# Optimization experiments

Measured on AMD Instinct MI355X. Metric: run time of the kernel, lower is better.

## Reference

```python
import jax, jax.numpy as jnp
import numpy as np

T1 = 0.2
T2 = 1.2
LABEL_SMOOTHING = 0.05
NUM_ITERS = 20  # fixed-point iterations for lambda_t_a (t2 > 1 branch)


def log_t(x, t):
    # tempered log (t != 1)
    return (x ** (1.0 - t) - 1.0) / (1.0 - t)


def exp_t(x, t):
    # tempered exp (t != 1): relu((1-t)x + 1) ** (1/(1-t))
    return jnp.maximum((1.0 - t) * x + 1.0, 0.0) ** (1.0 / (1.0 - t))


def lambda_t_a(a, t):
    # t > 1 fixed-point branch of the original torch code, with a fixed
    # iteration count instead of a host-synced convergence check.
    mu = jnp.max(a, axis=-1, keepdims=True)            # [N, 1]
    norm_a_initial = a - mu                            # [N, C], <= 0

    def body(norm_a, _):
        z_a = jnp.sum(exp_t(norm_a, t), axis=-1, keepdims=True)  # [N, 1]
        return z_a ** (1.0 - t) * norm_a_initial, None

    norm_a, _ = jax.lax.scan(body, norm_a_initial, None, length=NUM_ITERS)
    z_a = jnp.sum(exp_t(norm_a, t), axis=-1, keepdims=True)
    return -log_t(1.0 / z_a, t) + mu                   # [N, 1]


def setup_inputs() -> dict:
    key = jax.random.key(0)
    k1, k2 = jax.random.split(key)
    N, C = 16384, 1000
    inputs = jax.random.normal(k1, (N, C), dtype=jnp.float32)
    labels = jax.random.randint(k2, (N,), 0, C)
    targets = jax.nn.one_hot(labels, C, dtype=jnp.float32)
    return {"inputs": inputs, "targets": targets}


def reference(inputs, targets):
    num_classes = targets.shape[-1]
    # label smoothing (label_smoothing > 0 branch)
    targets = (1.0 - num_classes / (num_classes - 1) * LABEL_SMOOTHING) * targets \
              + LABEL_SMOOTHING / (num_classes - 1)
    norm_constants = lambda_t_a(inputs, T2)                      # [N, 1]
    probabilities = exp_t(inputs - norm_constants, T2)           # [N, C]
    loss1 = targets * (log_t(targets + 1e-8, T1) - log_t(probabilities, T1))
    loss2 = (targets ** (2.0 - T1) - probabilities ** (2.0 - T1)) / (2.0 - T1)
    out = jnp.sum(loss1 - loss2, axis=-1)                        # [N]
    return jnp.mean(out)
```

## Files before the change

### kernel.cpp

```cpp
#include <hip/hip_runtime.h>
#include <math.h>

#define C_DIM 1000
#define BIG   1.0e30f

__device__ __forceinline__ float fexp2(float x) { return __builtin_amdgcn_exp2f(x); }
__device__ __forceinline__ float flog2(float x) { return __builtin_amdgcn_logf(x); }
__device__ __forceinline__ float frcp(float x)  { return __builtin_amdgcn_rcpf(x); }

template <int CTRL, int RM>
__device__ __forceinline__ float dpp_add_term(float x) {
    int y = __builtin_amdgcn_update_dpp(0, __float_as_int(x), CTRL, RM, 0xf, true);
    return __int_as_float(y);
}
template <int CTRL, int RM>
__device__ __forceinline__ float dpp_max_term(float x) {
    int y = __builtin_amdgcn_update_dpp(__float_as_int(x), __float_as_int(x), CTRL, RM, 0xf, false);
    return __int_as_float(y);
}

#define DPP_SUM_CHAIN(x)                      \
    x += dpp_add_term<0x111, 0xf>(x);         \
    x += dpp_add_term<0x112, 0xf>(x);         \
    x += dpp_add_term<0x114, 0xf>(x);         \
    x += dpp_add_term<0x118, 0xf>(x);         \
    x += dpp_add_term<0x142, 0xa>(x);         \
    x += dpp_add_term<0x143, 0xc>(x);

__device__ __forceinline__ float bcast63(float x) {
    return __int_as_float(__builtin_amdgcn_readlane(__float_as_int(x), 63));
}

__device__ __forceinline__ float wave_sum(float x) {
    DPP_SUM_CHAIN(x)
    return bcast63(x);
}

__device__ __forceinline__ float wave_max(float x) {
    x = fmaxf(x, dpp_max_term<0x111, 0xf>(x));
    x = fmaxf(x, dpp_max_term<0x112, 0xf>(x));
    x = fmaxf(x, dpp_max_term<0x114, 0xf>(x));
    x = fmaxf(x, dpp_max_term<0x118, 0xf>(x));
    x = fmaxf(x, dpp_max_term<0x142, 0xa>(x));
    x = fmaxf(x, dpp_max_term<0x143, 0xc>(x));
    return bcast63(x);
}

__device__ __forceinline__ float tr16(const float4 x0, const float4 x1,
                                      const float4 x2, const float4 x3,
                                      float bb[16])
{
    bb[0]=-0.2f*x0.x;  bb[1]=-0.2f*x0.y;  bb[2]=-0.2f*x0.z;  bb[3]=-0.2f*x0.w;
    bb[4]=-0.2f*x1.x;  bb[5]=-0.2f*x1.y;  bb[6]=-0.2f*x1.z;  bb[7]=-0.2f*x1.w;
    bb[8]=-0.2f*x2.x;  bb[9]=-0.2f*x2.y;  bb[10]=-0.2f*x2.z; bb[11]=-0.2f*x2.w;
    bb[12]=-0.2f*x3.x; bb[13]=-0.2f*x3.y; bb[14]=-0.2f*x3.z; bb[15]=-0.2f*x3.w;
    float m0 = fmaxf(fmaxf(x0.x, x0.y), fmaxf(x0.z, x0.w));
    float m1 = fmaxf(fmaxf(x1.x, x1.y), fmaxf(x1.z, x1.w));
    float m2 = fmaxf(fmaxf(x2.x, x2.y), fmaxf(x2.z, x2.w));
    float m3 = fmaxf(fmaxf(x3.x, x3.y), fmaxf(x3.z, x3.w));
    return fmaxf(fmaxf(m0, m1), fmaxf(m2, m3));
}

__device__ __forceinline__ float dot16(const float4 t0, const float4 t1,
                                       const float4 t2, const float4 t3,
                                       const float bb[16])
{
    float s = 0.0f;
    s = fmaf(t0.x, bb[0],  s); s = fmaf(t0.y, bb[1],  s);
    s = fmaf(t0.z, bb[2],  s); s = fmaf(t0.w, bb[3],  s);
    s = fmaf(t1.x, bb[4],  s); s = fmaf(t1.y, bb[5],  s);
    s = fmaf(t1.z, bb[6],  s); s = fmaf(t1.w, bb[7],  s);
    s = fmaf(t2.x, bb[8],  s); s = fmaf(t2.y, bb[9],  s);
    s = fmaf(t2.z, bb[10], s); s = fmaf(t2.w, bb[11], s);
    s = fmaf(t3.x, bb[12], s); s = fmaf(t3.y, bb[13], s);
    s = fmaf(t3.z, bb[14], s); s = fmaf(t3.w, bb[15], s);
    return s;
}

__device__ __forceinline__ void row_core(const float bb[16], float mxl, float ahbl,
                                         float* __restrict__ row_out, int row, int lane,
                                         float C0, float E_off, float dE)
{
    const float mu  = wave_max(mxl);
    const float ahb = wave_sum(ahbl);
    const float g   = 0.2f * mu;
    const float hb  = ahb + g;

    const float c1 = 1.0f + g;
    float s = 0.0f;
    #pragma unroll
    for (int k = 0; k < 16; ++k) {
        float u = bb[k] + c1;
        float u2 = u * u;
        s += frcp(u2 * u2 * u);
    }
    s = wave_sum(s);
    const float lam = fexp2(-0.2f * flog2(s));

    const float c2 = fmaf(lam, g, 1.0f);
    s = 0.0f;
    #pragma unroll
    for (int k = 0; k < 16; ++k) {
        float u = fmaf(lam, bb[k], c2);
        float u2 = u * u;
        s += frcp(u2 * u2 * u);
    }
    s = wave_sum(s);
    const float w = fexp2(0.2f * flog2(s));

    const float c3 = w + g;
    float S4 = 0.0f, S5 = 0.0f, S6 = 0.0f, S9 = 0.0f, S10 = 0.0f, S11 = 0.0f;
    #pragma unroll
    for (int k = 0; k < 16; ++k) {
        float r  = frcp(bb[k] + c3);
        float r2 = r * r;
        float r4 = r2 * r2;
        float r5 = r4 * r;
        float r9 = r4 * r5;
        S4  += r4;
        S5  += r5;
        S6  += r5 * r;
        S9  += r9;
        S10 += r5 * r5;
        S11 += r9 * r2;
    }
    DPP_SUM_CHAIN(S4)
    DPP_SUM_CHAIN(S5)
    DPP_SUM_CHAIN(S6)
    DPP_SUM_CHAIN(S9)
    DPP_SUM_CHAIN(S10)
    DPP_SUM_CHAIN(S11)
    S4 = bcast63(S4);  S5 = bcast63(S5);  S6 = bcast63(S6);
    S9 = bcast63(S9);  S10 = bcast63(S10); S11 = bcast63(S11);

    const float d   = (S5 - 1.0f) * 0.2f * frcp(S6);
    const float w1  = w + d;
    const float d2  = d * d;
    const float S4c = S4 + fmaf(10.0f * d2, S6,  -4.0f * d * S5);
    const float S9c = S9 + fmaf(45.0f * d2, S11, -9.0f * d * S10);
    const float rh  = frcp(w1 + hb);
    const float rh2 = rh * rh;
    const float rh4 = rh2 * rh2;

    const float loss = fmaf(-E_off, S4c,
                       fmaf(-dE, rh4,
                       fmaf(1.0f / 1.8f, S9c, C0)));
    if (lane == 0) row_out[row] = loss;
}

__global__ __launch_bounds__(256, 8) void btll(
    const float* __restrict__ inputs, const float* __restrict__ targets,
    float* __restrict__ row_out, int n_rows,
    float C0, float E_off, float dE)
{
    const int lane = threadIdx.x & 63;
    const int wave = threadIdx.x >> 6;
    const int wid  = blockIdx.x * 4 + wave;
    int row0 = wid * 2;
    if (row0 >= n_rows) return;
    int row1 = row0 + 1;
    const bool has1 = row1 < n_rows;
    if (!has1) row1 = row0;

    const float4* in0 = (const float4*)(inputs  + (size_t)row0 * C_DIM);
    const float4* tg0 = (const float4*)(targets + (size_t)row0 * C_DIM);
    const float4* in1 = (const float4*)(inputs  + (size_t)row1 * C_DIM);
    const float4* tg1 = (const float4*)(targets + (size_t)row1 * C_DIM);
    const bool m3 = (lane + 192) < 250;
    const float4 xpad = make_float4(-BIG, -BIG, -BIG, -BIG);
    const float4 tpad = make_float4(0.f, 0.f, 0.f, 0.f);

    float4 a0 = in0[lane];
    float4 a1 = in0[lane + 64];
    float4 a2 = in0[lane + 128];
    float4 a3 = m3 ? in0[lane + 192] : xpad;
    float4 t0 = tg0[lane];
    float4 t1 = tg0[lane + 64];
    float4 t2 = tg0[lane + 128];
    float4 t3 = m3 ? tg0[lane + 192] : tpad;
    float4 p0 = in1[lane];
    float4 p1 = in1[lane + 64];
    float4 p2 = in1[lane + 128];
    float4 p3 = m3 ? in1[lane + 192] : xpad;

    float bbA[16];
    float mxA = tr16(a0, a1, a2, a3, bbA);
    float ahA = dot16(t0, t1, t2, t3, bbA);

    float4 q0 = tg1[lane];
    float4 q1 = tg1[lane + 64];
    float4 q2 = tg1[lane + 128];
    float4 q3 = m3 ? tg1[lane + 192] : tpad;

    float bbB[16];
    float mxB = tr16(p0, p1, p2, p3, bbB);
    float ahB = dot16(q0, q1, q2, q3, bbB);

    row_core(bbA, mxA, ahA, row_out, row0, lane, C0, E_off, dE);
    if (has1) row_core(bbB, mxB, ahB, row_out, row1, lane, C0, E_off, dE);
}

__global__ __launch_bounds__(1024) void reduce_mean(
    const float* __restrict__ row_out, float* __restrict__ out, int n)
{
    __shared__ double sm[16];
    const int lane = threadIdx.x & 63;
    const int wv   = threadIdx.x >> 6;
    const int n4   = n >> 2;
    const float4* r4 = (const float4*)row_out;
    double s = 0.0;
    for (int i = threadIdx.x; i < n4; i += 1024) {
        float4 v = r4[i];
        s += (double)v.x + (double)v.y + (double)v.z + (double)v.w;
    }
    if (threadIdx.x == 0)
        for (int i = n4 << 2; i < n; ++i) s += (double)row_out[i];
    #pragma unroll
    for (int off = 32; off > 0; off >>= 1) s += __shfl_xor(s, off, 64);
    if (lane == 0) sm[wv] = s;
    __syncthreads();
    if (wv == 0) {
        double t = (lane < 16) ? sm[lane] : 0.0;
        #pragma unroll
        for (int off = 32; off > 0; off >>= 1) t += __shfl_xor(t, off, 64);
        if (lane == 0) out[0] = (float)(t / (double)n);
    }
}

extern "C" void kernel_launch(void* const* d_in, const int* in_sizes, int n_in,
                              void* d_out, int out_size, void* d_ws, size_t ws_size,
                              hipStream_t stream) {
    const float* inputs  = (const float*)d_in[0];
    const float* targets = (const float*)d_in[1];
    float* out = (float*)d_out;

    const int N = in_sizes[0] / C_DIM;
    float* row_out = (float*)d_ws;

    const double ls    = 0.05;
    const double c1g_d = 1.0 - (1000.0 / 999.0) * ls;
    const double c2_d  = ls / 999.0;
    const float  tp_on_f  = (float)c1g_d + (float)c2_d;
    const float  tp_off_f = (float)c2_d;
    const double tp_on  = (double)tp_on_f;
    const double tp_off = (double)tp_off_f;
    const double A_on  = (pow(tp_on  + 1e-8, 0.8) - 1.0) / 0.8;
    const double A_off = (pow(tp_off + 1e-8, 0.8) - 1.0) / 0.8;
    const double B_on  = pow(tp_on,  1.8);
    const double B_off = pow(tp_off, 1.8);
    const double E_on_d  = 1.25 * tp_on;
    const double E_off_d = 1.25 * tp_off;
    const double F_on_d  = tp_on  * A_on  + E_on_d  - B_on  / 1.8;
    const double F_off_d = tp_off * A_off + E_off_d - B_off / 1.8;
    const double C0_d    = (C_DIM - 1) * F_off_d + F_on_d;
    const double dE_d    = E_on_d - E_off_d;

    dim3 grid((N + 7) / 8);
    btll<<<grid, 256, 0, stream>>>(inputs, targets, row_out, N,
                                   (float)C0_d, (float)E_off_d, (float)dE_d);
    reduce_mean<<<1, 1024, 0, stream>>>(row_out, out, N);
}
```

Measured before the change: 168.6 us.

## Process four rows per wave with software-pipelined prefetch of next row

```diff
diff --git a/kernel.cpp b/kernel.cpp
--- a/kernel.cpp
+++ b/kernel.cpp
@@ -79,7 +79,7 @@
 
 __device__ __forceinline__ void row_core(const float bb[16], float mxl, float ahbl,
                                          float* __restrict__ row_out, int row, int lane,
-                                         float C0, float E_off, float dE)
+                                         bool st, float C0, float E_off, float dE)
 {
     const float mu  = wave_max(mxl);
     const float ahb = wave_sum(ahbl);
@@ -145,10 +145,10 @@
     const float loss = fmaf(-E_off, S4c,
                        fmaf(-dE, rh4,
                        fmaf(1.0f / 1.8f, S9c, C0)));
-    if (lane == 0) row_out[row] = loss;
-}
-
-__global__ __launch_bounds__(256, 8) void btll(
+    if (st && lane == 0) row_out[row] = loss;
+}
+
+__global__ __launch_bounds__(256, 4) void btll(
     const float* __restrict__ inputs, const float* __restrict__ targets,
     float* __restrict__ row_out, int n_rows,
     float C0, float E_off, float dE)
@@ -156,16 +156,26 @@
     const int lane = threadIdx.x & 63;
     const int wave = threadIdx.x >> 6;
     const int wid  = blockIdx.x * 4 + wave;
-    int row0 = wid * 2;
-    if (row0 >= n_rows) return;
-    int row1 = row0 + 1;
-    const bool has1 = row1 < n_rows;
-    if (!has1) row1 = row0;
-
-    const float4* in0 = (const float4*)(inputs  + (size_t)row0 * C_DIM);
-    const float4* tg0 = (const float4*)(targets + (size_t)row0 * C_DIM);
-    const float4* in1 = (const float4*)(inputs  + (size_t)row1 * C_DIM);
-    const float4* tg1 = (const float4*)(targets + (size_t)row1 * C_DIM);
+    const int rbase = wid * 4;
+    if (rbase >= n_rows) return;
+
+    const int r0 = rbase;
+    const int r1 = min(rbase + 1, n_rows - 1);
+    const int r2 = min(rbase + 2, n_rows - 1);
+    const int r3 = min(rbase + 3, n_rows - 1);
+    const bool st1 = (rbase + 1) < n_rows;
+    const bool st2 = (rbase + 2) < n_rows;
+    const bool st3 = (rbase + 3) < n_rows;
+
+    const float4* in0 = (const float4*)(inputs  + (size_t)r0 * C_DIM);
+    const float4* tg0 = (const float4*)(targets + (size_t)r0 * C_DIM);
+    const float4* in1 = (const float4*)(inputs  + (size_t)r1 * C_DIM);
+    const float4* tg1 = (const float4*)(targets + (size_t)r1 * C_DIM);
+    const float4* in2 = (const float4*)(inputs  + (size_t)r2 * C_DIM);
+    const float4* tg2 = (const float4*)(targets + (size_t)r2 * C_DIM);
+    const float4* in3 = (const float4*)(inputs  + (size_t)r3 * C_DIM);
+    const float4* tg3 = (const float4*)(targets + (size_t)r3 * C_DIM);
+
     const bool m3 = (lane + 192) < 250;
     const float4 xpad = make_float4(-BIG, -BIG, -BIG, -BIG);
     const float4 tpad = make_float4(0.f, 0.f, 0.f, 0.f);
@@ -183,21 +193,47 @@
     float4 p2 = in1[lane + 128];
     float4 p3 = m3 ? in1[lane + 192] : xpad;
 
-    float bbA[16];
-    float mxA = tr16(a0, a1, a2, a3, bbA);
-    float ahA = dot16(t0, t1, t2, t3, bbA);
-
-    float4 q0 = tg1[lane];
-    float4 q1 = tg1[lane + 64];
-    float4 q2 = tg1[lane + 128];
-    float4 q3 = m3 ? tg1[lane + 192] : tpad;
-
-    float bbB[16];
-    float mxB = tr16(p0, p1, p2, p3, bbB);
-    float ahB = dot16(q0, q1, q2, q3, bbB);
-
-    row_core(bbA, mxA, ahA, row_out, row0, lane, C0, E_off, dE);
-    if (has1) row_core(bbB, mxB, ahB, row_out, row1, lane, C0, E_off, dE);
+    float bbA[16], bbB[16];
+    float mx, ah;
+
+    mx = tr16(a0, a1, a2, a3, bbA);
+    ah = dot16(t0, t1, t2, t3, bbA);
+    t0 = tg1[lane];
+    t1 = tg1[lane + 64];
+    t2 = tg1[lane + 128];
+    t3 = m3 ? tg1[lane + 192] : tpad;
+
+    row_core(bbA, mx, ah, row_out, r0, lane, true, C0, E_off, dE);
+
+    mx = tr16(p0, p1, p2, p3, bbB);
+    ah = dot16(t0, t1, t2, t3, bbB);
+    p0 = in2[lane];
+    p1 = in2[lane + 64];
+    p2 = in2[lane + 128];
+    p3 = m3 ? in2[lane + 192] : xpad;
+    t0 = tg2[lane];
+    t1 = tg2[lane + 64];
+    t2 = tg2[lane + 128];
+    t3 = m3 ? tg2[lane + 192] : tpad;
+
+    row_core(bbB, mx, ah, row_out, r1, lane, st1, C0, E_off, dE);
+
+    mx = tr16(p0, p1, p2, p3, bbA);
+    ah = dot16(t0, t1, t2, t3, bbA);
+    p0 = in3[lane];
+    p1 = in3[lane + 64];
+    p2 = in3[lane + 128];
+    p3 = m3 ? in3[lane + 192] : xpad;
+    t0 = tg3[lane];
+    t1 = tg3[lane + 64];
+    t2 = tg3[lane + 128];
+    t3 = m3 ? tg3[lane + 192] : tpad;
+
+    row_core(bbA, mx, ah, row_out, r2, lane, st2, C0, E_off, dE);
+
+    mx = tr16(p0, p1, p2, p3, bbB);
+    ah = dot16(t0, t1, t2, t3, bbB);
+    row_core(bbB, mx, ah, row_out, r3, lane, st3, C0, E_off, dE);
 }
 
 __global__ __launch_bounds__(1024) void reduce_mean(
@@ -255,7 +291,7 @@
     const double C0_d    = (C_DIM - 1) * F_off_d + F_on_d;
     const double dE_d    = E_on_d - E_off_d;
 
-    dim3 grid((N + 7) / 8);
+    dim3 grid((N + 15) / 16);
     btll<<<grid, 256, 0, stream>>>(inputs, targets, row_out, N,
                                    (float)C0_d, (float)E_off_d, (float)dE_d);
     reduce_mean<<<1, 1024, 0, stream>>>(row_out, out, N);
```

New measurement: 148.6 us. 11.9% less time.

## Stage targets through LDS with async loads and prefetch second row

Applied to the files above, without the earlier changes.

```diff
diff --git a/kernel.cpp b/kernel.cpp
--- a/kernel.cpp
+++ b/kernel.cpp
@@ -1,12 +1,22 @@
 #include <hip/hip_runtime.h>
 #include <math.h>
+#include <stdint.h>
 
 #define C_DIM 1000
 #define BIG   1.0e30f
+
+typedef float fx4 __attribute__((ext_vector_type(4)));
+
+typedef __attribute__((address_space(1))) void g_void;
+typedef __attribute__((address_space(3))) void l_void;
 
 __device__ __forceinline__ float fexp2(float x) { return __builtin_amdgcn_exp2f(x); }
 __device__ __forceinline__ float flog2(float x) { return __builtin_amdgcn_logf(x); }
 __device__ __forceinline__ float frcp(float x)  { return __builtin_amdgcn_rcpf(x); }
+
+__device__ __forceinline__ void gll16(const float* g, float* l) {
+    __builtin_amdgcn_global_load_lds((g_void*)g, (l_void*)l, 16, 0, 0);
+}
 
 template <int CTRL, int RM>
 __device__ __forceinline__ float dpp_add_term(float x) {
@@ -46,8 +56,8 @@
     return bcast63(x);
 }
 
-__device__ __forceinline__ float tr16(const float4 x0, const float4 x1,
-                                      const float4 x2, const float4 x3,
+__device__ __forceinline__ float tr16(const fx4 x0, const fx4 x1,
+                                      const fx4 x2, const fx4 x3,
                                       float bb[16])
 {
     bb[0]=-0.2f*x0.x;  bb[1]=-0.2f*x0.y;  bb[2]=-0.2f*x0.z;  bb[3]=-0.2f*x0.w;
@@ -61,8 +71,8 @@
     return fmaxf(fmaxf(m0, m1), fmaxf(m2, m3));
 }
 
-__device__ __forceinline__ float dot16(const float4 t0, const float4 t1,
-                                       const float4 t2, const float4 t3,
+__device__ __forceinline__ float dot16(const fx4 t0, const fx4 t1,
+                                       const fx4 t2, const fx4 t3,
                                        const float bb[16])
 {
     float s = 0.0f;
@@ -79,7 +89,7 @@
 
 __device__ __forceinline__ void row_core(const float bb[16], float mxl, float ahbl,
                                          float* __restrict__ row_out, int row, int lane,
-                                         float C0, float E_off, float dE)
+                                         bool st, float C0, float E_off, float dE)
 {
     const float mu  = wave_max(mxl);
     const float ahb = wave_sum(ahbl);
@@ -145,7 +155,7 @@
     const float loss = fmaf(-E_off, S4c,
                        fmaf(-dE, rh4,
                        fmaf(1.0f / 1.8f, S9c, C0)));
-    if (lane == 0) row_out[row] = loss;
+    if (st && lane == 0) row_out[row] = loss;
 }
 
 __global__ __launch_bounds__(256, 8) void btll(
@@ -156,48 +166,77 @@
     const int lane = threadIdx.x & 63;
     const int wave = threadIdx.x >> 6;
     const int wid  = blockIdx.x * 4 + wave;
-    int row0 = wid * 2;
-    if (row0 >= n_rows) return;
-    int row1 = row0 + 1;
-    const bool has1 = row1 < n_rows;
-    if (!has1) row1 = row0;
-
-    const float4* in0 = (const float4*)(inputs  + (size_t)row0 * C_DIM);
-    const float4* tg0 = (const float4*)(targets + (size_t)row0 * C_DIM);
-    const float4* in1 = (const float4*)(inputs  + (size_t)row1 * C_DIM);
-    const float4* tg1 = (const float4*)(targets + (size_t)row1 * C_DIM);
-    const bool m3 = (lane + 192) < 250;
-    const float4 xpad = make_float4(-BIG, -BIG, -BIG, -BIG);
-    const float4 tpad = make_float4(0.f, 0.f, 0.f, 0.f);
-
-    float4 a0 = in0[lane];
-    float4 a1 = in0[lane + 64];
-    float4 a2 = in0[lane + 128];
-    float4 a3 = m3 ? in0[lane + 192] : xpad;
-    float4 t0 = tg0[lane];
-    float4 t1 = tg0[lane + 64];
-    float4 t2 = tg0[lane + 128];
-    float4 t3 = m3 ? tg0[lane + 192] : tpad;
-    float4 p0 = in1[lane];
-    float4 p1 = in1[lane + 64];
-    float4 p2 = in1[lane + 128];
-    float4 p3 = m3 ? in1[lane + 192] : xpad;
-
-    float bbA[16];
-    float mxA = tr16(a0, a1, a2, a3, bbA);
-    float ahA = dot16(t0, t1, t2, t3, bbA);
-
-    float4 q0 = tg1[lane];
-    float4 q1 = tg1[lane + 64];
-    float4 q2 = tg1[lane + 128];
-    float4 q3 = m3 ? tg1[lane + 192] : tpad;
-
-    float bbB[16];
-    float mxB = tr16(p0, p1, p2, p3, bbB);
-    float ahB = dot16(q0, q1, q2, q3, bbB);
-
-    row_core(bbA, mxA, ahA, row_out, row0, lane, C0, E_off, dE);
-    if (has1) row_core(bbB, mxB, ahB, row_out, row1, lane, C0, E_off, dE);
+    const int r0i  = wid * 2;
+    if (r0i >= n_rows) return;
+    int r1i = r0i + 1;
+    const bool st1 = r1i < n_rows;
+    if (!st1) r1i = r0i;
+
+    __shared__ __align__(16) float ldsT[4][1024];
+    float* lt = &ldsT[wave][0];
+
+    const float* in0 = inputs  + (size_t)r0i * C_DIM;
+    const float* tg0 = targets + (size_t)r0i * C_DIM;
+    const float* in1 = inputs  + (size_t)r1i * C_DIM;
+    const float* tg1 = targets + (size_t)r1i * C_DIM;
+
+    const bool m3 = lane < 58;
+    const int  o3 = m3 ? (768 + 4 * lane) : 0;
+    const fx4  xpad = (fx4){-BIG, -BIG, -BIG, -BIG};
+    const fx4  zero = (fx4){0.f, 0.f, 0.f, 0.f};
+
+    fx4 x0 = *(const fx4*)(in0 + 4 * lane);
+    fx4 x1 = *(const fx4*)(in0 + 256 + 4 * lane);
+    fx4 x2 = *(const fx4*)(in0 + 512 + 4 * lane);
+    fx4 x3 = *(const fx4*)(in0 + o3);
+    gll16(tg0 + 4 * lane,       lt);
+    gll16(tg0 + 256 + 4 * lane, lt + 256);
+    gll16(tg0 + 512 + 4 * lane, lt + 512);
+    gll16(tg0 + o3,             lt + 768);
+
+    x3 = m3 ? x3 : xpad;
+    float bbA[16], bbB[16];
+    float mx = tr16(x0, x1, x2, x3, bbA);
+
+    asm volatile("s_waitcnt vmcnt(0)" ::: "memory");
+    fx4 tv0 = *(const fx4*)(lt + 4 * lane);
+    fx4 tv1 = *(const fx4*)(lt + 256 + 4 * lane);
+    fx4 tv2 = *(const fx4*)(lt + 512 + 4 * lane);
+    fx4 tv3 = *(const fx4*)(lt + 768 + 4 * lane);
+    tv3 = m3 ? tv3 : zero;
+    float ah = dot16(tv0, tv1, tv2, tv3, bbA);
+
+    gll16(tg1 + 4 * lane,       lt);
+    gll16(tg1 + 256 + 4 * lane, lt + 256);
+    gll16(tg1 + 512 + 4 * lane, lt + 512);
+    gll16(tg1 + o3,             lt + 768);
+    fx4 p0, p1, p2, p3;
+    {
+        const float* a0 = in1 + 4 * lane;
+        const float* a1 = in1 + 256 + 4 * lane;
+        const float* a2 = in1 + 512 + 4 * lane;
+        const float* a3 = in1 + o3;
+        asm volatile("global_load_dwordx4 %0, %1, off" : "=v"(p0) : "v"(a0));
+        asm volatile("global_load_dwordx4 %0, %1, off" : "=v"(p1) : "v"(a1));
+        asm volatile("global_load_dwordx4 %0, %1, off" : "=v"(p2) : "v"(a2));
+        asm volatile("global_load_dwordx4 %0, %1, off" : "=v"(p3) : "v"(a3));
+    }
+    asm volatile("" ::: "memory");
+
+    row_core(bbA, mx, ah, row_out, r0i, lane, true, C0, E_off, dE);
+
+    asm volatile("s_waitcnt vmcnt(1)"
+                 : "+v"(p0), "+v"(p1), "+v"(p2), "+v"(p3) :: "memory");
+    p3 = m3 ? p3 : xpad;
+    mx = tr16(p0, p1, p2, p3, bbB);
+    tv0 = *(const fx4*)(lt + 4 * lane);
+    tv1 = *(const fx4*)(lt + 256 + 4 * lane);
+    tv2 = *(const fx4*)(lt + 512 + 4 * lane);
+    tv3 = *(const fx4*)(lt + 768 + 4 * lane);
+    tv3 = m3 ? tv3 : zero;
+    ah = dot16(tv0, tv1, tv2, tv3, bbB);
+
+    row_core(bbB, mx, ah, row_out, r1i, lane, st1, C0, E_off, dE);
 }
 
 __global__ __launch_bounds__(1024) void reduce_mean(
```

Result: faster. 146.5 us (-13.1%).
